# Optimization experiments

Hardware: AMD Instinct MI355X
Metric: run time of the kernel (lower is better)

The kernel has to match this reference:

```python
import jax, jax.numpy as jnp
import numpy as np

DEPTH, DIM, DFF, VOCAB = 4, 512, 2048, 4096
EPS = 1e-5

def layernorm(x, w, b):
    mu = jnp.mean(x, axis=-1, keepdims=True)
    var = jnp.mean((x - mu) ** 2, axis=-1, keepdims=True)
    return (x - mu) * jax.lax.rsqrt(var + EPS) * w + b

def sconv(x, phazor_c, last_conv_c):
    # x: [B,L,dim] real; phazor_c, last_conv_c: [dim] complex
    B, L, D = x.shape
    r = jnp.abs(phazor_c)
    p = jnp.tanh(r) * jnp.exp(1j * jnp.angle(phazor_c))          # [dim]
    prog = p[None, :] ** jnp.arange(L, dtype=jnp.float32)[:, None]  # [L,dim]
    filt_fft = jnp.fft.fft(prog, n=2 * L, axis=0)                # [2L,dim]
    x_fft = jnp.fft.fft(x.astype(jnp.complex64), n=2 * L, axis=1)  # [B,2L,dim]
    conv = jnp.fft.ifft(filt_fft[None] * x_fft, axis=1)[:, :L]   # [B,L,dim]
    conv = conv + last_conv_c[None, None, :] * prog[None] * p[None, None, :]
    return conv.real.astype(x.dtype)

def setup_inputs() -> dict:
    key = jax.random.key(0)
    ks = jax.random.split(key, 20)
    f32 = jnp.float32
    inp = {}
    inp['x'] = jax.random.normal(ks[0], (2, 4096, VOCAB), dtype=f32)
    inp['Win'] = jax.random.normal(ks[1], (DIM, VOCAB), dtype=f32) * VOCAB ** -0.5
    inp['bin'] = jnp.zeros((DIM,), f32)
    inp['ln1_w'] = jnp.ones((DEPTH, DIM), f32)
    inp['ln1_b'] = jnp.zeros((DEPTH, DIM), f32)
    # phazor init: exp(2*pi*i*arange/dim)*|randn|
    ang = 2 * np.pi * jnp.arange(DIM, dtype=f32) / DIM
    mag = jnp.abs(jax.random.normal(ks[2], (DEPTH, DIM), dtype=f32))
    inp['phz_re'] = mag * jnp.cos(ang)[None]
    inp['phz_im'] = mag * jnp.sin(ang)[None]
    inp['lc_re'] = jax.random.normal(ks[3], (DEPTH, DIM), dtype=f32)
    inp['lc_im'] = jax.random.normal(ks[4], (DEPTH, DIM), dtype=f32)
    inp['sc_lin'] = jnp.ones((DEPTH, DIM), f32)
    inp['ln2_w'] = jnp.ones((DEPTH, DIM), f32)
    inp['ln2_b'] = jnp.zeros((DEPTH, DIM), f32)
    inp['W1'] = jax.random.normal(ks[5], (DEPTH, DFF, DIM), dtype=f32) * DIM ** -0.5
    inp['b1'] = jnp.zeros((DEPTH, DFF), f32)
    inp['W2'] = jax.random.normal(ks[6], (DEPTH, DIM, DFF), dtype=f32) * DFF ** -0.5
    inp['b2'] = jnp.zeros((DEPTH, DIM), f32)
    inp['lnl_w'] = jnp.ones((DIM,), f32)
    inp['lnl_b'] = jnp.zeros((DIM,), f32)
    inp['Wout'] = jax.random.normal(ks[7], (VOCAB, DIM), dtype=f32) * DIM ** -0.5
    inp['bout'] = jnp.zeros((VOCAB,), f32)
    return inp

def _forward(x, Win, bin, ln1_w, ln1_b, phz_re, phz_im, lc_re, lc_im, sc_lin,
             ln2_w, ln2_b, W1, b1, W2, b2, lnl_w, lnl_b, Wout, bout):
    h = jnp.einsum('blv,dv->bld', x, Win) + bin  # token_in

    def body(h, p):
        l1w, l1b, pr, pi, lr, li, scl, l2w, l2b, w1, b1_, w2, b2_ = p
        y = jax.nn.silu(layernorm(h, l1w, l1b))
        y = sconv(y, pr + 1j * pi, lr + 1j * li)
        h = h + y * scl
        y = layernorm(h, l2w, l2b)
        y = jax.nn.silu(jnp.einsum('bld,fd->blf', y, w1) + b1_)
        y = jnp.einsum('blf,df->bld', y, w2) + b2_
        return h + y, None

    xs = (ln1_w, ln1_b, phz_re, phz_im, lc_re, lc_im, sc_lin,
          ln2_w, ln2_b, W1, b1, W2, b2)
    h, _ = jax.lax.scan(body, h, xs)
    h = layernorm(h, lnl_w, lnl_b)
    return jnp.einsum('bld,vd->blv', h, Wout) + bout

def reference(x, Win, bin, ln1_w, ln1_b, phz_re, phz_im, lc_re, lc_im, sc_lin,
              ln2_w, ln2_b, W1, b1, W2, b2, lnl_w, lnl_b, Wout, bout):
    return _forward(x, Win, bin, ln1_w, ln1_b, phz_re, phz_im, lc_re, lc_im,
                    sc_lin, ln2_w, ln2_b, W1, b1, W2, b2, lnl_w, lnl_b, Wout, bout)
```

## Files before the change

### kernel.cpp

```cpp
#include <hip/hip_runtime.h>
#include <hip/hip_bf16.h>
#include <cstdint>
#include <cstddef>

#define DEPTH 4
#define DIM 512
#define DFF 2048
#define VOCAB 4096
#define NB 2
#define LSEQ 4096
#define MR (NB*LSEQ)
#define EPSL 1e-5f
#define NC 256
#define TCH 16

typedef __attribute__((ext_vector_type(8))) short  s8v;
typedef __attribute__((ext_vector_type(4))) float  f4v;
typedef __attribute__((ext_vector_type(8))) __bf16 bf8v;

__device__ __forceinline__ unsigned short f2b(float f) {
  union { float f; unsigned int u; } v; v.f = f;
  unsigned int r = v.u + 0x7FFFu + ((v.u >> 16) & 1u);
  return (unsigned short)(r >> 16);
}

__device__ __forceinline__ void gld16(const void* g, void* l) {
  __builtin_amdgcn_global_load_lds(
      (const __attribute__((address_space(1))) unsigned int*)(uintptr_t)g,
      (__attribute__((address_space(3))) unsigned int*)(uintptr_t)l,
      16, 0, 0);
}

template<int N> __device__ __forceinline__ void wvm() {
  if constexpr (N == 8)      asm volatile("s_waitcnt vmcnt(8)" ::: "memory");
  else if constexpr (N == 4) asm volatile("s_waitcnt vmcnt(4)" ::: "memory");
  else                       asm volatile("s_waitcnt vmcnt(0)" ::: "memory");
}

__device__ __forceinline__ void wred64(float& s, float& s2) {
#pragma unroll
  for (int off = 32; off; off >>= 1) { s += __shfl_xor(s, off, 64); s2 += __shfl_xor(s2, off, 64); }
}

__global__ void __launch_bounds__(256) cvt_f32_bf16(
    const float* __restrict__ in, unsigned short* __restrict__ out, int n8)
{
  int i = blockIdx.x * 256 + threadIdx.x;
  if (i >= n8) return;
  const f4v* p = (const f4v*)(in + (size_t)i * 8);
  f4v a = p[0], b = p[1];
  s8v o;
  o[0]=(short)f2b(a[0]); o[1]=(short)f2b(a[1]); o[2]=(short)f2b(a[2]); o[3]=(short)f2b(a[3]);
  o[4]=(short)f2b(b[0]); o[5]=(short)f2b(b[1]); o[6]=(short)f2b(b[2]); o[7]=(short)f2b(b[3]);
  *(s8v*)(out + (size_t)i * 8) = o;
}

__device__ __forceinline__ void phz2p(float re, float im, float& pre, float& pim) {
  float r = sqrtf(re * re + im * im);
  float t = (r > 1e-20f) ? (tanhf(r) / r) : 1.0f;
  pre = t * re; pim = t * im;
}

template<int RES>
__global__ void __launch_bounds__(512) red_ln_scan(
    const float* __restrict__ parts, float* __restrict__ h, const float* __restrict__ bias,
    const float* __restrict__ lnw, const float* __restrict__ lnb,
    const float* __restrict__ pr, const float* __restrict__ pi,
    float* __restrict__ y, float* __restrict__ stA)
{
  __shared__ float ls[TCH][DIM];
  const int d = threadIdx.x;
  const int c = blockIdx.x, b = blockIdx.y;
  const size_t rbase = ((size_t)b * LSEQ + (size_t)c * TCH) * DIM + d;
  const size_t st = (size_t)MR * DIM;
  const float bv = bias[d];
#pragma unroll 4
  for (int j = 0; j < TCH; ++j) {
    size_t o = rbase + (size_t)j * DIM;
    float v = parts[o] + parts[st + o] + parts[2 * st + o] + parts[3 * st + o] + bv;
    if (RES) v += h[o];
    h[o] = v;
    ls[j][d] = v;
  }
  __syncthreads();
  const int wave = threadIdx.x >> 6, lane = threadIdx.x & 63;
  const int c8 = lane * 8;
  f4v w0 = *(const f4v*)(lnw + c8), w1 = *(const f4v*)(lnw + c8 + 4);
  f4v b0 = *(const f4v*)(lnb + c8), b1 = *(const f4v*)(lnb + c8 + 4);
#pragma unroll
  for (int jj = 0; jj < 2; ++jj) {
    int j = wave * 2 + jj;
    f4v v0 = *(const f4v*)&ls[j][c8];
    f4v v1 = *(const f4v*)&ls[j][c8 + 4];
    float s = 0.f, s2 = 0.f;
#pragma unroll
    for (int q = 0; q < 4; ++q) { s += v0[q]; s2 += v0[q]*v0[q]; s += v1[q]; s2 += v1[q]*v1[q]; }
    wred64(s, s2);
    float mu = s * (1.f / DIM);
    float rs = rsqrtf(s2 * (1.f / DIM) - mu * mu + EPSL);
    f4v o0, o1;
#pragma unroll
    for (int q = 0; q < 4; ++q) {
      float a = (v0[q] - mu) * rs * w0[q] + b0[q];
      o0[q] = a / (1.f + __expf(-a));
      float e = (v1[q] - mu) * rs * w1[q] + b1[q];
      o1[q] = e / (1.f + __expf(-e));
    }
    *(f4v*)&ls[j][c8]     = o0;
    *(f4v*)&ls[j][c8 + 4] = o1;
    size_t yo = ((size_t)b * LSEQ + (size_t)c * TCH + j) * DIM + c8;
    *(f4v*)(y + yo)     = o0;
    *(f4v*)(y + yo + 4) = o1;
  }
  __syncthreads();
  float pre, pim; phz2p(pr[d], pi[d], pre, pim);
  float sre = 0.f, sim = 0.f;
#pragma unroll
  for (int j = 0; j < TCH; ++j) {
    float xv = ls[j][d];
    float nre = fmaf(pre, sre, fmaf(-pim, sim, xv));
    float nim = fmaf(pre, sim, pim * sre);
    sre = nre; sim = nim;
  }
  size_t o = (((size_t)b * NC + c) * DIM + d) * 2;
  stA[o] = sre; stA[o + 1] = sim;
}

__global__ void __launch_bounds__(256) scan_b(
    const float* __restrict__ stA, float* __restrict__ carry,
    const float* __restrict__ pr, const float* __restrict__ pi,
    const float* __restrict__ lcr, const float* __restrict__ lci)
{
  int idx = blockIdx.x * 256 + threadIdx.x;
  int b = idx >> 9, d = idx & (DIM - 1);
  float pre, pim; phz2p(pr[d], pi[d], pre, pim);
  float qre = pre, qim = pim;
#pragma unroll
  for (int t = 0; t < 4; ++t) { float nr = qre*qre - qim*qim; float ni = 2.f*qre*qim; qre = nr; qim = ni; }
  float cre = lcr[d], cim = lci[d];
#pragma unroll 4
  for (int c = 0; c < NC; ++c) {
    size_t o = (((size_t)b * NC + c) * DIM + d) * 2;
    carry[o] = cre; carry[o + 1] = cim;
    float are = stA[o], aim = stA[o + 1];
    float nr = fmaf(qre, cre, fmaf(-qim, cim, are));
    float ni = fmaf(qre, cim, fmaf(qim, cre, aim));
    cre = nr; cim = ni;
  }
}

__global__ void __launch_bounds__(512) scan_c_ln2(
    const float* __restrict__ y, float* __restrict__ h, const float* __restrict__ carry,
    const float* __restrict__ pr, const float* __restrict__ pi,
    const float* __restrict__ scl,
    const float* __restrict__ lnw, const float* __restrict__ lnb,
    unsigned short* __restrict__ yb)
{
  __shared__ float ls[TCH][DIM];
  const int d = threadIdx.x;
  const int c = blockIdx.x, b = blockIdx.y;
  float pre, pim; phz2p(pr[d], pi[d], pre, pim);
  size_t co = (((size_t)b * NC + c) * DIM + d) * 2;
  float sre = carry[co], sim = carry[co + 1];
  const float sc = scl[d];
  const size_t rbase = ((size_t)b * LSEQ + (size_t)c * TCH) * DIM + d;
#pragma unroll 4
  for (int j = 0; j < TCH; ++j) {
    size_t o = rbase + (size_t)j * DIM;
    float xv = y[o];
    float nre = fmaf(pre, sre, fmaf(-pim, sim, xv));
    float nim = fmaf(pre, sim, pim * sre);
    sre = nre; sim = nim;
    float hv = h[o] + sre * sc;
    h[o] = hv;
    ls[j][d] = hv;
  }
  __syncthreads();
  const int wave = threadIdx.x >> 6, lane = threadIdx.x & 63;
  const int c8 = lane * 8;
  f4v w0 = *(const f4v*)(lnw + c8), w1 = *(const f4v*)(lnw + c8 + 4);
  f4v b0 = *(const f4v*)(lnb + c8), b1 = *(const f4v*)(lnb + c8 + 4);
#pragma unroll
  for (int jj = 0; jj < 2; ++jj) {
    int j = wave * 2 + jj;
    f4v v0 = *(const f4v*)&ls[j][c8];
    f4v v1 = *(const f4v*)&ls[j][c8 + 4];
    float s = 0.f, s2 = 0.f;
#pragma unroll
    for (int q = 0; q < 4; ++q) { s += v0[q]; s2 += v0[q]*v0[q]; s += v1[q]; s2 += v1[q]*v1[q]; }
    wred64(s, s2);
    float mu = s * (1.f / DIM);
    float rs = rsqrtf(s2 * (1.f / DIM) - mu * mu + EPSL);
    s8v o;
#pragma unroll
    for (int q = 0; q < 4; ++q) {
      o[q]     = (short)f2b((v0[q] - mu) * rs * w0[q] + b0[q]);
      o[4 + q] = (short)f2b((v1[q] - mu) * rs * w1[q] + b1[q]);
    }
    *(s8v*)(yb + ((size_t)b * LSEQ + (size_t)c * TCH + j) * DIM + c8) = o;
  }
}

__global__ void __launch_bounds__(512) red_ln_final(
    const float* __restrict__ parts, const float* __restrict__ h, const float* __restrict__ bias,
    const float* __restrict__ lnw, const float* __restrict__ lnb,
    unsigned short* __restrict__ yb)
{
  __shared__ float ls[TCH][DIM];
  const int d = threadIdx.x;
  const int c = blockIdx.x, b = blockIdx.y;
  const size_t rbase = ((size_t)b * LSEQ + (size_t)c * TCH) * DIM + d;
  const size_t st = (size_t)MR * DIM;
  const float bv = bias[d];
#pragma unroll 4
  for (int j = 0; j < TCH; ++j) {
    size_t o = rbase + (size_t)j * DIM;
    float v = parts[o] + parts[st + o] + parts[2 * st + o] + parts[3 * st + o] + bv + h[o];
    ls[j][d] = v;
  }
  __syncthreads();
  const int wave = threadIdx.x >> 6, lane = threadIdx.x & 63;
  const int c8 = lane * 8;
  f4v w0 = *(const f4v*)(lnw + c8), w1 = *(const f4v*)(lnw + c8 + 4);
  f4v b0 = *(const f4v*)(lnb + c8), b1 = *(const f4v*)(lnb + c8 + 4);
#pragma unroll
  for (int jj = 0; jj < 2; ++jj) {
    int j = wave * 2 + jj;
    f4v v0 = *(const f4v*)&ls[j][c8];
    f4v v1 = *(const f4v*)&ls[j][c8 + 4];
    float s = 0.f, s2 = 0.f;
#pragma unroll
    for (int q = 0; q < 4; ++q) { s += v0[q]; s2 += v0[q]*v0[q]; s += v1[q]; s2 += v1[q]*v1[q]; }
    wred64(s, s2);
    float mu = s * (1.f / DIM);
    float rs = rsqrtf(s2 * (1.f / DIM) - mu * mu + EPSL);
    s8v o;
#pragma unroll
    for (int q = 0; q < 4; ++q) {
      o[q]     = (short)f2b((v0[q] - mu) * rs * w0[q] + b0[q]);
      o[4 + q] = (short)f2b((v1[q] - mu) * rs * w1[q] + b1[q]);
    }
    *(s8v*)(yb + ((size_t)b * LSEQ + (size_t)c * TCH + j) * DIM + c8) = o;
  }
}

template<int EPI>
__global__ void __launch_bounds__(256, 3) gemm_p(
    const unsigned short* __restrict__ A, const unsigned short* __restrict__ Bm,
    const float* __restrict__ bias,
    float* __restrict__ Cf, unsigned short* __restrict__ Cb,
    int N, int Keff, int lda, int ldb)
{
  __shared__ unsigned short As[3][128 * 32];
  __shared__ unsigned short Bs[3][128 * 32];
  const int tid  = threadIdx.x;
  const int lane = tid & 63, wave = tid >> 6;
  const int wm = wave >> 1, wn = wave & 1;
  const int fr = lane & 15, fq = lane >> 4;
  const int bz = blockIdx.z;

  int bx, by;
  {
    int gx = gridDim.x;
    int nwg = gx * gridDim.y;
    int b = blockIdx.y * gx + blockIdx.x;
    int lid = (b & 7) * (nwg >> 3) + (b >> 3);
    bx = lid % gx; by = lid / gx;
  }
  const int m0 = by * 128, n0 = bx * 128;
  const int koff = bz * Keff;
  const int nkt = Keff >> 5;

  f4v acc[4][4];
#pragma unroll
  for (int i = 0; i < 4; ++i)
#pragma unroll
    for (int j = 0; j < 4; ++j) acc[i][j] = (f4v){0.f, 0.f, 0.f, 0.f};

  const int row2 = tid >> 2, col2 = (tid & 3) << 3;
  auto stage = [&](int buf, int kt) {
    const unsigned short* Ab = A  + (size_t)m0 * lda + koff + kt * 32;
    const unsigned short* Bb = Bm + (size_t)n0 * ldb + koff + kt * 32;
    gld16(Ab + (size_t)row2 * lda + col2,        &As[buf][tid * 8]);
    gld16(Ab + (size_t)(row2 + 64) * lda + col2, &As[buf][(256 + tid) * 8]);
    gld16(Bb + (size_t)row2 * ldb + col2,        &Bs[buf][tid * 8]);
    gld16(Bb + (size_t)(row2 + 64) * ldb + col2, &Bs[buf][(256 + tid) * 8]);
  };

  stage(0, 0);
  stage(1, 1);

  int b0 = 0, b1 = 1, b2 = 2;
  for (int kt = 0; kt < nkt; ++kt) {
    bool pf = (kt + 2 < nkt);
    if (pf) stage(b2, kt + 2);
    if (pf)                    wvm<8>();
    else if (kt + 1 < nkt)     wvm<4>();
    else                       wvm<0>();
    __builtin_amdgcn_s_barrier();
    __builtin_amdgcn_sched_barrier(0);
    bf8v av[4], bv[4];
#pragma unroll
    for (int i = 0; i < 4; ++i)
      av[i] = *(const bf8v*)&As[b0][(wm * 64 + i * 16 + fr) * 32 + fq * 8];
#pragma unroll
    for (int j = 0; j < 4; ++j)
      bv[j] = *(const bf8v*)&Bs[b0][(wn * 64 + j * 16 + fr) * 32 + fq * 8];
#pragma unroll
    for (int i = 0; i < 4; ++i)
#pragma unroll
      for (int j = 0; j < 4; ++j)
        acc[i][j] = __builtin_amdgcn_mfma_f32_16x16x32_bf16(av[i], bv[j], acc[i][j], 0, 0, 0);
    __builtin_amdgcn_sched_barrier(0);
    __builtin_amdgcn_s_barrier();
    int t = b0; b0 = b1; b1 = b2; b2 = t;
  }

  const size_t pbase = (EPI == 3) ? (size_t)bz * MR * N : 0;
#pragma unroll
  for (int j = 0; j < 4; ++j) {
    const int col = n0 + wn * 64 + j * 16 + fr;
    const float bsv = (EPI == 3) ? 0.f : bias[col];
#pragma unroll
    for (int i = 0; i < 4; ++i) {
#pragma unroll
      for (int r = 0; r < 4; ++r) {
        const int row = m0 + wm * 64 + i * 16 + fq * 4 + r;
        const size_t off = (size_t)row * N + col;
        float v = acc[i][j][r] + bsv;
        if constexpr (EPI == 0) {
          Cf[off] = v;
        } else if constexpr (EPI == 1) {
          float sv = v / (1.f + __expf(-v));
          Cb[off] = f2b(sv);
        } else {
          Cf[pbase + off] = v;
        }
      }
    }
  }
}

extern "C" void kernel_launch(void* const* d_in, const int* in_sizes, int n_in,
                              void* d_out, int out_size, void* d_ws, size_t ws_size,
                              hipStream_t stream)
{
  (void)in_sizes; (void)n_in; (void)out_size; (void)ws_size;
  const float* x    = (const float*)d_in[0];
  const float* Win  = (const float*)d_in[1];
  const float* bin  = (const float*)d_in[2];
  const float* ln1w = (const float*)d_in[3];
  const float* ln1b = (const float*)d_in[4];
  const float* phzr = (const float*)d_in[5];
  const float* phzi = (const float*)d_in[6];
  const float* lcr  = (const float*)d_in[7];
  const float* lci  = (const float*)d_in[8];
  const float* scl  = (const float*)d_in[9];
  const float* ln2w = (const float*)d_in[10];
  const float* ln2b = (const float*)d_in[11];
  const float* W1   = (const float*)d_in[12];
  const float* b1   = (const float*)d_in[13];
  const float* W2   = (const float*)d_in[14];
  const float* b2   = (const float*)d_in[15];
  const float* lnlw = (const float*)d_in[16];
  const float* lnlb = (const float*)d_in[17];
  const float* Wout = (const float*)d_in[18];
  const float* bout = (const float*)d_in[19];

  char* wsp = (char*)d_ws;
  auto alloc = [&](size_t bytes) { char* p = wsp; wsp += (bytes + 255) & ~(size_t)255; return p; };
  float*          h     = (float*)alloc((size_t)MR * DIM * 4);
  float*          y     = (float*)alloc((size_t)MR * DIM * 4);
  unsigned short* yb    = (unsigned short*)alloc((size_t)MR * DIM * 2);
  unsigned short* Winb  = (unsigned short*)alloc((size_t)DIM * VOCAB * 2);
  unsigned short* W1b   = (unsigned short*)alloc((size_t)DEPTH * DFF * DIM * 2);
  unsigned short* W2b   = (unsigned short*)alloc((size_t)DEPTH * DIM * DFF * 2);
  unsigned short* Woutb = (unsigned short*)alloc((size_t)VOCAB * DIM * 2);
  float*          stA   = (float*)alloc((size_t)NB * NC * DIM * 2 * 4);
  float*          carry = (float*)alloc((size_t)NB * NC * DIM * 2 * 4);

  unsigned short* xb    = (unsigned short*)d_out;
  unsigned short* act1  = (unsigned short*)d_out;
  float*          parts = (float*)((char*)d_out + ((size_t)64 << 20));

  dim3 blk(256);
  dim3 fblk(512);
  dim3 fgrid(NC, NB);
  cvt_f32_bf16<<<dim3(((size_t)MR * VOCAB) / 2048), blk, 0, stream>>>(x, xb, (int)(((size_t)MR * VOCAB) / 8));
  cvt_f32_bf16<<<dim3((DIM * VOCAB) / 2048), blk, 0, stream>>>(Win, Winb, DIM * VOCAB / 8);
  cvt_f32_bf16<<<dim3((DEPTH * DFF * DIM) / 2048), blk, 0, stream>>>(W1, W1b, DEPTH * DFF * DIM / 8);
  cvt_f32_bf16<<<dim3((DEPTH * DFF * DIM) / 2048), blk, 0, stream>>>(W2, W2b, DEPTH * DIM * DFF / 8);
  cvt_f32_bf16<<<dim3((VOCAB * DIM) / 2048), blk, 0, stream>>>(Wout, Woutb, VOCAB * DIM / 8);

  gemm_p<3><<<dim3(DIM / 128, MR / 128, 4), blk, 0, stream>>>(
      xb, Winb, nullptr, parts, nullptr, DIM, VOCAB / 4, VOCAB, VOCAB);
  red_ln_scan<0><<<fgrid, fblk, 0, stream>>>(parts, h, bin, ln1w, ln1b, phzr, phzi, y, stA);

  for (int l = 0; l < DEPTH; ++l) {
    scan_b<<<dim3((NB * DIM) / 256), blk, 0, stream>>>(stA, carry, phzr + l * DIM, phzi + l * DIM,
                                                       lcr + l * DIM, lci + l * DIM);
    scan_c_ln2<<<fgrid, fblk, 0, stream>>>(y, h, carry, phzr + l * DIM, phzi + l * DIM,
                                           scl + l * DIM, ln2w + l * DIM, ln2b + l * DIM, yb);
    gemm_p<1><<<dim3(DFF / 128, MR / 128, 1), blk, 0, stream>>>(
        yb, W1b + (size_t)l * DFF * DIM, b1 + l * DFF, nullptr, act1, DFF, DIM, DIM, DIM);
    gemm_p<3><<<dim3(DIM / 128, MR / 128, 4), blk, 0, stream>>>(
        act1, W2b + (size_t)l * DIM * DFF, nullptr, parts, nullptr, DIM, DFF / 4, DFF, DFF);
    if (l < DEPTH - 1) {
      red_ln_scan<1><<<fgrid, fblk, 0, stream>>>(parts, h, b2 + l * DIM,
                                                 ln1w + (l + 1) * DIM, ln1b + (l + 1) * DIM,
                                                 phzr + (l + 1) * DIM, phzi + (l + 1) * DIM, y, stA);
    }
  }
  red_ln_final<<<fgrid, fblk, 0, stream>>>(parts, h, b2 + (DEPTH - 1) * DIM, lnlw, lnlb, yb);
  gemm_p<0><<<dim3(VOCAB / 128, MR / 128, 1), blk, 0, stream>>>(
      yb, Woutb, bout, (float*)d_out, nullptr, VOCAB, DIM, DIM, DIM);
}
```

Measured before the change: 661.1 us.

## Replace split-K partial sums with BN=64 GEMM tiles writing residual directly

The narrow N=512 GEMMs (token-in and W2) no longer use 4-way split-K with partial buffers that a later kernel reduces. They instead use a 128x64 tile variant with full K and add bias plus residual straight into h in the epilogue. The LayerNorm kernels then just read h, which removes the four-way partial read and the parts buffer traffic. scan_b also batches its stA loads eight at a time so the loads overlap. The trade-off is fewer blocks per GEMM, each with a longer K loop, which may lower parallelism on the N=512 GEMMs.

```diff
diff --git a/kernel.cpp b/kernel.cpp
--- a/kernel.cpp
+++ b/kernel.cpp
@@ -33,7 +33,9 @@
 
 template<int N> __device__ __forceinline__ void wvm() {
   if constexpr (N == 8)      asm volatile("s_waitcnt vmcnt(8)" ::: "memory");
+  else if constexpr (N == 6) asm volatile("s_waitcnt vmcnt(6)" ::: "memory");
   else if constexpr (N == 4) asm volatile("s_waitcnt vmcnt(4)" ::: "memory");
+  else if constexpr (N == 3) asm volatile("s_waitcnt vmcnt(3)" ::: "memory");
   else                       asm volatile("s_waitcnt vmcnt(0)" ::: "memory");
 }
 
@@ -61,9 +63,8 @@
   pre = t * re; pim = t * im;
 }
 
-template<int RES>
-__global__ void __launch_bounds__(512) red_ln_scan(
-    const float* __restrict__ parts, float* __restrict__ h, const float* __restrict__ bias,
+__global__ void __launch_bounds__(512) ln_scan(
+    const float* __restrict__ h,
     const float* __restrict__ lnw, const float* __restrict__ lnb,
     const float* __restrict__ pr, const float* __restrict__ pi,
     float* __restrict__ y, float* __restrict__ stA)
@@ -72,16 +73,8 @@
   const int d = threadIdx.x;
   const int c = blockIdx.x, b = blockIdx.y;
   const size_t rbase = ((size_t)b * LSEQ + (size_t)c * TCH) * DIM + d;
-  const size_t st = (size_t)MR * DIM;
-  const float bv = bias[d];
 #pragma unroll 4
-  for (int j = 0; j < TCH; ++j) {
-    size_t o = rbase + (size_t)j * DIM;
-    float v = parts[o] + parts[st + o] + parts[2 * st + o] + parts[3 * st + o] + bv;
-    if (RES) v += h[o];
-    h[o] = v;
-    ls[j][d] = v;
-  }
+  for (int j = 0; j < TCH; ++j) ls[j][d] = h[rbase + (size_t)j * DIM];
   __syncthreads();
   const int wave = threadIdx.x >> 6, lane = threadIdx.x & 63;
   const int c8 = lane * 8;
@@ -138,14 +131,22 @@
 #pragma unroll
   for (int t = 0; t < 4; ++t) { float nr = qre*qre - qim*qim; float ni = 2.f*qre*qim; qre = nr; qim = ni; }
   float cre = lcr[d], cim = lci[d];
-#pragma unroll 4
-  for (int c = 0; c < NC; ++c) {
-    size_t o = (((size_t)b * NC + c) * DIM + d) * 2;
-    carry[o] = cre; carry[o + 1] = cim;
-    float are = stA[o], aim = stA[o + 1];
-    float nr = fmaf(qre, cre, fmaf(-qim, cim, are));
-    float ni = fmaf(qre, cim, fmaf(qim, cre, aim));
-    cre = nr; cim = ni;
+  const size_t base = (size_t)b * NC * DIM * 2 + (size_t)d * 2;
+  for (int c0 = 0; c0 < NC; c0 += 8) {
+    float ar[8], ai[8];
+#pragma unroll
+    for (int k = 0; k < 8; ++k) {
+      size_t o = base + (size_t)(c0 + k) * DIM * 2;
+      ar[k] = stA[o]; ai[k] = stA[o + 1];
+    }
+#pragma unroll
+    for (int k = 0; k < 8; ++k) {
+      size_t o = base + (size_t)(c0 + k) * DIM * 2;
+      carry[o] = cre; carry[o + 1] = cim;
+      float nr = fmaf(qre, cre, fmaf(-qim, cim, ar[k]));
+      float ni = fmaf(qre, cim, fmaf(qim, cre, ai[k]));
+      cre = nr; cim = ni;
+    }
   }
 }
 
@@ -201,8 +202,8 @@
   }
 }
 
-__global__ void __launch_bounds__(512) red_ln_final(
-    const float* __restrict__ parts, const float* __restrict__ h, const float* __restrict__ bias,
+__global__ void __launch_bounds__(512) ln_final(
+    const float* __restrict__ h,
     const float* __restrict__ lnw, const float* __restrict__ lnb,
     unsigned short* __restrict__ yb)
 {
@@ -210,14 +211,8 @@
   const int d = threadIdx.x;
   const int c = blockIdx.x, b = blockIdx.y;
   const size_t rbase = ((size_t)b * LSEQ + (size_t)c * TCH) * DIM + d;
-  const size_t st = (size_t)MR * DIM;
-  const float bv = bias[d];
 #pragma unroll 4
-  for (int j = 0; j < TCH; ++j) {
-    size_t o = rbase + (size_t)j * DIM;
-    float v = parts[o] + parts[st + o] + parts[2 * st + o] + parts[3 * st + o] + bv + h[o];
-    ls[j][d] = v;
-  }
+  for (int j = 0; j < TCH; ++j) ls[j][d] = h[rbase + (size_t)j * DIM];
   __syncthreads();
   const int wave = threadIdx.x >> 6, lane = threadIdx.x & 63;
   const int c8 = lane * 8;
@@ -244,20 +239,22 @@
   }
 }
 
-template<int EPI>
-__global__ void __launch_bounds__(256, 3) gemm_p(
+template<int EPI, int BN>
+__global__ void __launch_bounds__(256, BN == 64 ? 4 : 3) gemm_p(
     const unsigned short* __restrict__ A, const unsigned short* __restrict__ Bm,
     const float* __restrict__ bias,
     float* __restrict__ Cf, unsigned short* __restrict__ Cb,
-    int N, int Keff, int lda, int ldb)
-{
+    int N, int K, int lda, int ldb)
+{
+  constexpr int WN  = BN / 2;
+  constexpr int NJ  = WN / 16;
+  constexpr int VPT = 2 + BN / 64;
   __shared__ unsigned short As[3][128 * 32];
-  __shared__ unsigned short Bs[3][128 * 32];
+  __shared__ unsigned short Bs[3][BN * 32];
   const int tid  = threadIdx.x;
   const int lane = tid & 63, wave = tid >> 6;
   const int wm = wave >> 1, wn = wave & 1;
   const int fr = lane & 15, fq = lane >> 4;
-  const int bz = blockIdx.z;
 
   int bx, by;
   {
@@ -267,24 +264,24 @@
     int lid = (b & 7) * (nwg >> 3) + (b >> 3);
     bx = lid % gx; by = lid / gx;
   }
-  const int m0 = by * 128, n0 = bx * 128;
-  const int koff = bz * Keff;
-  const int nkt = Keff >> 5;
-
-  f4v acc[4][4];
+  const int m0 = by * 128, n0 = bx * BN;
+  const int nkt = K >> 5;
+
+  f4v acc[4][NJ];
 #pragma unroll
   for (int i = 0; i < 4; ++i)
 #pragma unroll
-    for (int j = 0; j < 4; ++j) acc[i][j] = (f4v){0.f, 0.f, 0.f, 0.f};
+    for (int j = 0; j < NJ; ++j) acc[i][j] = (f4v){0.f, 0.f, 0.f, 0.f};
 
   const int row2 = tid >> 2, col2 = (tid & 3) << 3;
   auto stage = [&](int buf, int kt) {
-    const unsigned short* Ab = A  + (size_t)m0 * lda + koff + kt * 32;
-    const unsigned short* Bb = Bm + (size_t)n0 * ldb + koff + kt * 32;
+    const unsigned short* Ab = A  + (size_t)m0 * lda + kt * 32;
+    const unsigned short* Bb = Bm + (size_t)n0 * ldb + kt * 32;
     gld16(Ab + (size_t)row2 * lda + col2,        &As[buf][tid * 8]);
     gld16(Ab + (size_t)(row2 + 64) * lda + col2, &As[buf][(256 + tid) * 8]);
     gld16(Bb + (size_t)row2 * ldb + col2,        &Bs[buf][tid * 8]);
-    gld16(Bb + (size_t)(row2 + 64) * ldb + col2, &Bs[buf][(256 + tid) * 8]);
+    if constexpr (BN == 128)
+      gld16(Bb + (size_t)(row2 + 64) * ldb + col2, &Bs[buf][(256 + tid) * 8]);
   };
 
   stage(0, 0);
@@ -294,33 +291,32 @@
   for (int kt = 0; kt < nkt; ++kt) {
     bool pf = (kt + 2 < nkt);
     if (pf) stage(b2, kt + 2);
-    if (pf)                    wvm<8>();
-    else if (kt + 1 < nkt)     wvm<4>();
+    if (pf)                    wvm<2 * VPT>();
+    else if (kt + 1 < nkt)     wvm<VPT>();
     else                       wvm<0>();
     __builtin_amdgcn_s_barrier();
     __builtin_amdgcn_sched_barrier(0);
-    bf8v av[4], bv[4];
+    bf8v av[4], bv[NJ];
 #pragma unroll
     for (int i = 0; i < 4; ++i)
       av[i] = *(const bf8v*)&As[b0][(wm * 64 + i * 16 + fr) * 32 + fq * 8];
 #pragma unroll
-    for (int j = 0; j < 4; ++j)
-      bv[j] = *(const bf8v*)&Bs[b0][(wn * 64 + j * 16 + fr) * 32 + fq * 8];
+    for (int j = 0; j < NJ; ++j)
+      bv[j] = *(const bf8v*)&Bs[b0][(wn * WN + j * 16 + fr) * 32 + fq * 8];
 #pragma unroll
     for (int i = 0; i < 4; ++i)
 #pragma unroll
-      for (int j = 0; j < 4; ++j)
+      for (int j = 0; j < NJ; ++j)
         acc[i][j] = __builtin_amdgcn_mfma_f32_16x16x32_bf16(av[i], bv[j], acc[i][j], 0, 0, 0);
     __builtin_amdgcn_sched_barrier(0);
     __builtin_amdgcn_s_barrier();
     int t = b0; b0 = b1; b1 = b2; b2 = t;
   }
 
-  const size_t pbase = (EPI == 3) ? (size_t)bz * MR * N : 0;
-#pragma unroll
-  for (int j = 0; j < 4; ++j) {
-    const int col = n0 + wn * 64 + j * 16 + fr;
-    const float bsv = (EPI == 3) ? 0.f : bias[col];
+#pragma unroll
+  for (int j = 0; j < NJ; ++j) {
+    const int col = n0 + wn * WN + j * 16 + fr;
+    const float bsv = bias[col];
 #pragma unroll
     for (int i = 0; i < 4; ++i) {
 #pragma unroll
@@ -334,7 +330,7 @@
           float sv = v / (1.f + __expf(-v));
           Cb[off] = f2b(sv);
         } else {
-          Cf[pbase + off] = v;
+          Cf[off] = Cf[off] + v;
         }
       }
     }
@@ -379,9 +375,8 @@
   float*          stA   = (float*)alloc((size_t)NB * NC * DIM * 2 * 4);
   float*          carry = (float*)alloc((size_t)NB * NC * DIM * 2 * 4);
 
-  unsigned short* xb    = (unsigned short*)d_out;
-  unsigned short* act1  = (unsigned short*)d_out;
-  float*          parts = (float*)((char*)d_out + ((size_t)64 << 20));
+  unsigned short* xb   = (unsigned short*)d_out;
+  unsigned short* act1 = (unsigned short*)d_out;
 
   dim3 blk(256);
   dim3 fblk(512);
@@ -392,26 +387,25 @@
   cvt_f32_bf16<<<dim3((DEPTH * DFF * DIM) / 2048), blk, 0, stream>>>(W2, W2b, DEPTH * DIM * DFF / 8);
   cvt_f32_bf16<<<dim3((VOCAB * DIM) / 2048), blk, 0, stream>>>(Wout, Woutb, VOCAB * DIM / 8);
 
-  gemm_p<3><<<dim3(DIM / 128, MR / 128, 4), blk, 0, stream>>>(
-      xb, Winb, nullptr, parts, nullptr, DIM, VOCAB / 4, VOCAB, VOCAB);
-  red_ln_scan<0><<<fgrid, fblk, 0, stream>>>(parts, h, bin, ln1w, ln1b, phzr, phzi, y, stA);
+  gemm_p<0, 64><<<dim3(DIM / 64, MR / 128), blk, 0, stream>>>(
+      xb, Winb, bin, h, nullptr, DIM, VOCAB, VOCAB, VOCAB);
+  ln_scan<<<fgrid, fblk, 0, stream>>>(h, ln1w, ln1b, phzr, phzi, y, stA);
 
   for (int l = 0; l < DEPTH; ++l) {
     scan_b<<<dim3((NB * DIM) / 256), blk, 0, stream>>>(stA, carry, phzr + l * DIM, phzi + l * DIM,
                                                        lcr + l * DIM, lci + l * DIM);
     scan_c_ln2<<<fgrid, fblk, 0, stream>>>(y, h, carry, phzr + l * DIM, phzi + l * DIM,
                                            scl + l * DIM, ln2w + l * DIM, ln2b + l * DIM, yb);
-    gemm_p<1><<<dim3(DFF / 128, MR / 128, 1), blk, 0, stream>>>(
+    gemm_p<1, 128><<<dim3(DFF / 128, MR / 128), blk, 0, stream>>>(
         yb, W1b + (size_t)l * DFF * DIM, b1 + l * DFF, nullptr, act1, DFF, DIM, DIM, DIM);
-    gemm_p<3><<<dim3(DIM / 128, MR / 128, 4), blk, 0, stream>>>(
-        act1, W2b + (size_t)l * DIM * DFF, nullptr, parts, nullptr, DIM, DFF / 4, DFF, DFF);
+    gemm_p<2, 64><<<dim3(DIM / 64, MR / 128), blk, 0, stream>>>(
+        act1, W2b + (size_t)l * DIM * DFF, b2 + l * DIM, h, nullptr, DIM, DFF, DFF, DFF);
     if (l < DEPTH - 1) {
-      red_ln_scan<1><<<fgrid, fblk, 0, stream>>>(parts, h, b2 + l * DIM,
-                                                 ln1w + (l + 1) * DIM, ln1b + (l + 1) * DIM,
-                                                 phzr + (l + 1) * DIM, phzi + (l + 1) * DIM, y, stA);
-    }
-  }
-  red_ln_final<<<fgrid, fblk, 0, stream>>>(parts, h, b2 + (DEPTH - 1) * DIM, lnlw, lnlb, yb);
-  gemm_p<0><<<dim3(VOCAB / 128, MR / 128, 1), blk, 0, stream>>>(
+      ln_scan<<<fgrid, fblk, 0, stream>>>(h, ln1w + (l + 1) * DIM, ln1b + (l + 1) * DIM,
+                                          phzr + (l + 1) * DIM, phzi + (l + 1) * DIM, y, stA);
+    }
+  }
+  ln_final<<<fgrid, fblk, 0, stream>>>(h, lnlw, lnlb, yb);
+  gemm_p<0, 128><<<dim3(VOCAB / 128, MR / 128), blk, 0, stream>>>(
       yb, Woutb, bout, (float*)d_out, nullptr, VOCAB, DIM, DIM, DIM);
 }
```

Result: faster. 584.3 us (-11.6%).
